# Kernel tuning notes

Measured on AMD Instinct MI355X. Metric: run time of the kernel, lower is better.

Reference implementation:

```python
import jax, jax.numpy as jnp
import numpy as np

NUM_HEADS = 32
ROPE_BASE = 10000.0
MASK_NEG = -66504.0  # from (1 - tril) * -66504.0 in the source


def _rotate_half(x):
    d = x.shape[-1] // 2
    return jnp.concatenate([-x[..., d:], x[..., :d]], axis=-1)


def setup_inputs() -> dict:
    key = jax.random.key(0)
    k1, k2, k3, k4 = jax.random.split(key, 4)
    S, B, E = 2048, 2, 2048
    return {
        "hidden_states": jax.random.normal(k1, (S, B, E), dtype=jnp.float32) * 0.02,
        "qkv_w": jax.random.normal(k2, (E, 3 * E), dtype=jnp.float32) * 0.02,
        "qkv_b": jax.random.normal(k3, (3 * E,), dtype=jnp.float32) * 0.02,
        "out_w": jax.random.normal(k4, (E, E), dtype=jnp.float32) * 0.02,
        "out_b": jnp.zeros((E,), dtype=jnp.float32),
    }


def reference(hidden_states, qkv_w, qkv_b, out_w, out_b):
    # seq-first prompt/prefill path of IPEXTransformerAtten
    S, B, E = hidden_states.shape
    H = NUM_HEADS
    D = E // H

    # fused QKV projection (mm_qkv_out)
    qkv = jnp.einsum('sbe,ef->sbf', hidden_states, qkv_w) + qkv_b  # [S,B,3E]
    q, k, v = jnp.split(qkv, 3, axis=-1)
    q = q.reshape(S, B, H, D)
    k = k.reshape(S, B, H, D)
    v = v.reshape(S, B, H, D)

    # rotary embedding (GPT-NeoX style, full head_dim)
    inv_freq = 1.0 / (ROPE_BASE ** (jnp.arange(0, D, 2, dtype=jnp.float32) / D))
    freqs = jnp.arange(S, dtype=jnp.float32)[:, None] * inv_freq  # [S, D/2]
    emb = jnp.concatenate([freqs, freqs], axis=-1)  # [S, D]
    cos = jnp.cos(emb)[:, None, None, :].astype(hidden_states.dtype)
    sin = jnp.sin(emb)[:, None, None, :].astype(hidden_states.dtype)
    q = q * cos + _rotate_half(q) * sin
    k = k * cos + _rotate_half(k) * sin

    # scaled dot-product attention with causal mask
    scale = 1.0 / jnp.sqrt(jnp.array(D, dtype=hidden_states.dtype))
    scores = jnp.einsum('sbhd,tbhd->bhst', q, k) * scale  # [B,H,S,S]
    causal = jnp.tril(jnp.ones((S, S), dtype=scores.dtype))
    scores = scores + (1.0 - causal) * MASK_NEG
    attn = jax.nn.softmax(scores, axis=-1)
    ctx = jnp.einsum('bhst,tbhd->sbhd', attn, v).reshape(S, B, E)

    # output projection
    return jnp.einsum('sbe,ef->sbf', ctx, out_w) + out_b
```

## Files before the change

### kernel.cpp

```cpp
#include <hip/hip_runtime.h>
#include <hip/hip_bf16.h>

#define S_LEN 2048
#define BATCH 2
#define EMB   2048
#define NH    32
#define HD    64
#define M_ROWS (S_LEN * BATCH)
#define QKV_N  (3 * EMB)

typedef short bf16x8 __attribute__((ext_vector_type(8)));
typedef float f32x4  __attribute__((ext_vector_type(4)));

__device__ __forceinline__ unsigned short f2bf(float f) {
  unsigned int u = __float_as_uint(f);
  u += 0x7fffu + ((u >> 16) & 1u);
  return (unsigned short)(u >> 16);
}
__device__ __forceinline__ float bf2f(unsigned short h) {
  return __uint_as_float(((unsigned int)h) << 16);
}
__device__ __forceinline__ void async_copy16(const void* g, void* lds_d) {
  __builtin_amdgcn_global_load_lds(
      (const __attribute__((address_space(1))) void*)g,
      (__attribute__((address_space(3))) void*)lds_d, 16, 0, 0);
}

#if __has_builtin(__builtin_amdgcn_exp2f)
#define EXP2F(x) __builtin_amdgcn_exp2f(x)
#else
#define EXP2F(x) __expf((x) * 0.6931471805599453f)
#endif


__global__ __launch_bounds__(256) void cast_to_bf16(
    const float* __restrict__ in, unsigned short* __restrict__ out, int n4) {
  int i = blockIdx.x * 256 + threadIdx.x;
  if (i >= n4) return;
  float4 v = reinterpret_cast<const float4*>(in)[i];
  ushort4 o;
  o.x = f2bf(v.x); o.y = f2bf(v.y); o.z = f2bf(v.z); o.w = f2bf(v.w);
  reinterpret_cast<ushort4*>(out)[i] = o;
}

__global__ __launch_bounds__(256) void transpose_cast(
    const float* __restrict__ in, unsigned short* __restrict__ out, int R, int C) {
  __shared__ unsigned short t[64][65];
  const int bc = blockIdx.x * 64, br = blockIdx.y * 64;
  const int tx = threadIdx.x & 63, ty = threadIdx.x >> 6;
  #pragma unroll
  for (int rr = ty; rr < 64; rr += 4)
    t[rr][tx] = f2bf(in[(size_t)(br + rr) * C + bc + tx]);
  __syncthreads();
  #pragma unroll
  for (int rr = ty; rr < 64; rr += 4)
    out[(size_t)(bc + rr) * R + br + tx] = t[tx][rr];
}


constexpr int TILE_SH = 24576;
constexpr int GEMM_LDS_BYTES = 3 * TILE_SH * 2;

__global__ __launch_bounds__(512, 2) void gemm_qkv(
    const unsigned short* __restrict__ A,
    const unsigned short* __restrict__ Wt,
    const float* __restrict__ bias,
    unsigned short* __restrict__ Qo,
    unsigned short* __restrict__ Ko,
    unsigned short* __restrict__ Vo) {
  extern __shared__ unsigned short lds[];
  const int tid = threadIdx.x;
  const int n0 = blockIdx.x * 128;
  const int m0 = blockIdx.y * 256;
  const int wave = tid >> 6, lane = tid & 63;
  const int wm = (wave >> 1) * 64, wn = (wave & 1) * 64;
  const int lm = lane & 15, lq = lane >> 4;
  const int K = 2048;
  const int NT = K / 64;

  const int srow = tid >> 3;
  const int gch  = (tid & 7) ^ (srow & 7);
  const unsigned short* Ab = A  + (size_t)(m0 + srow) * K + gch * 8;
  const unsigned short* Bb = Wt + (size_t)(n0 + srow) * K + gch * 8;

  auto stA = [&](int bufi, int k0, int rep) {
    async_copy16(Ab + (size_t)rep * 64 * K + k0,
                 lds + (size_t)bufi * TILE_SH + ((size_t)rep * 512 + tid) * 8);
  };
  auto stB = [&](int bufi, int k0, int rep) {
    async_copy16(Bb + (size_t)rep * 64 * K + k0,
                 lds + (size_t)bufi * TILE_SH + 16384 + ((size_t)rep * 512 + tid) * 8);
  };

  f32x4 acc[4][4] = {};

  stA(0, 0, 0); stA(0, 0, 1); stA(0, 0, 2); stA(0, 0, 3); stB(0, 0, 0); stB(0, 0, 1);
  stA(1, 64, 0); stA(1, 64, 1); stA(1, 64, 2); stA(1, 64, 3); stB(1, 64, 0); stB(1, 64, 1);
  asm volatile("s_waitcnt vmcnt(6)" ::: "memory");
  __builtin_amdgcn_s_barrier();

  int cur = 0;
  for (int t = 0; t < NT; t++) {
    const unsigned short* Abuf = lds + (size_t)cur * TILE_SH;
    const unsigned short* Bbuf = Abuf + 16384;
    const int pb = (cur >= 1) ? cur - 1 : 2;
    const int pk = (t + 2) * 64;
    const bool pre = (t + 2) < NT;

    bf16x8 b[4][2], a[2][2];
    #pragma unroll
    for (int j = 0; j < 4; j++) {
      const int R = wn + j * 16 + lm;
      #pragma unroll
      for (int ks = 0; ks < 2; ks++)
        b[j][ks] = *reinterpret_cast<const bf16x8*>(
            Bbuf + (size_t)R * 64 + (((ks * 4 + lq) ^ (R & 7)) * 8));
    }
    #pragma unroll
    for (int i = 0; i < 2; i++) {
      const int R = wm + i * 16 + lm;
      #pragma unroll
      for (int ks = 0; ks < 2; ks++)
        a[i][ks] = *reinterpret_cast<const bf16x8*>(
            Abuf + (size_t)R * 64 + (((ks * 4 + lq) ^ (R & 7)) * 8));
    }
    if (pre) { stA(pb, pk, 0); stA(pb, pk, 1); stB(pb, pk, 0); }
    __builtin_amdgcn_s_barrier();
    asm volatile("s_waitcnt lgkmcnt(0)" ::: "memory");
    __builtin_amdgcn_s_setprio(1);
    #pragma unroll
    for (int ks = 0; ks < 2; ks++)
      #pragma unroll
      for (int i = 0; i < 2; i++)
        #pragma unroll
        for (int j = 0; j < 4; j++)
          acc[i][j] = __builtin_amdgcn_mfma_f32_16x16x32_bf16(a[i][ks], b[j][ks], acc[i][j], 0, 0, 0);
    __builtin_amdgcn_s_setprio(0);
    __builtin_amdgcn_s_barrier();

    #pragma unroll
    for (int i = 0; i < 2; i++) {
      const int R = wm + (i + 2) * 16 + lm;
      #pragma unroll
      for (int ks = 0; ks < 2; ks++)
        a[i][ks] = *reinterpret_cast<const bf16x8*>(
            Abuf + (size_t)R * 64 + (((ks * 4 + lq) ^ (R & 7)) * 8));
    }
    if (pre) { stA(pb, pk, 2); stA(pb, pk, 3); stB(pb, pk, 1); }
    __builtin_amdgcn_s_barrier();
    asm volatile("s_waitcnt lgkmcnt(0)" ::: "memory");
    __builtin_amdgcn_s_setprio(1);
    #pragma unroll
    for (int ks = 0; ks < 2; ks++)
      #pragma unroll
      for (int i = 0; i < 2; i++)
        #pragma unroll
        for (int j = 0; j < 4; j++)
          acc[i + 2][j] = __builtin_amdgcn_mfma_f32_16x16x32_bf16(a[i][ks], b[j][ks], acc[i + 2][j], 0, 0, 0);
    __builtin_amdgcn_s_setprio(0);
    if (t + 1 < NT) {
      if (pre) asm volatile("s_waitcnt vmcnt(6)" ::: "memory");
      else     asm volatile("s_waitcnt vmcnt(0)" ::: "memory");
      __builtin_amdgcn_s_barrier();
    }
    cur = (cur == 2) ? 0 : cur + 1;
  }

  const int which = n0 >> 11;
  unsigned short* dst = (which == 0) ? Qo : (which == 1) ? Ko : Vo;
  float bv[4];
  #pragma unroll
  for (int j = 0; j < 4; j++) bv[j] = bias[n0 + wn + j * 16 + lm];

  if (which < 2) {
    #pragma unroll
    for (int j = 0; j < 2; j++) {
      const int n = n0 + wn + j * 16 + lm;
      const int e = n & (EMB - 1), h = e >> 6, d = e & 63;
      const float invf = EXP2F((float)d * -0.4152410118609203f);
      #pragma unroll
      for (int i = 0; i < 4; i++) {
        #pragma unroll
        for (int r = 0; r < 4; r++) {
          const int m = m0 + wm + i * 16 + lq * 4 + r;
          const int s = m >> 1, b = m & 1;
          const float v1 = acc[i][j][r]     + bv[j];
          const float v2 = acc[i][j + 2][r] + bv[j + 2];
          float sn, cs;
          __sincosf((float)s * invf, &sn, &cs);
          const size_t base = (((size_t)b * NH + h) * S_LEN + s) * HD + d;
          dst[base]      = f2bf(v1 * cs - v2 * sn);
          dst[base + 32] = f2bf(v2 * cs + v1 * sn);
        }
      }
    }
  } else {
    #pragma unroll
    for (int j = 0; j < 4; j++) {
      const int n = n0 + wn + j * 16 + lm;
      const int e = n & (EMB - 1), h = e >> 6, d = e & 63;
      #pragma unroll
      for (int i = 0; i < 4; i++) {
        #pragma unroll
        for (int r = 0; r < 4; r++) {
          const int m = m0 + wm + i * 16 + lq * 4 + r;
          const int s = m >> 1, b = m & 1;
          dst[(((size_t)b * NH + h) * S_LEN + s) * HD + d] = f2bf(acc[i][j][r] + bv[j]);
        }
      }
    }
  }
}


__global__ __launch_bounds__(256) void transpose_v(
    const unsigned short* __restrict__ V, unsigned short* __restrict__ VT) {
  __shared__ unsigned short t[64][65];
  const int bh = blockIdx.y;
  const int s0 = blockIdx.x * 64;
  const int tx = threadIdx.x & 63, ty = threadIdx.x >> 6;
  const unsigned short* src = V + ((size_t)bh * S_LEN + s0) * HD;
  #pragma unroll
  for (int r = ty; r < 64; r += 4)
    t[r][tx] = src[(size_t)r * HD + tx];
  __syncthreads();
  unsigned short* dst = VT + (size_t)bh * HD * S_LEN + s0;
  #pragma unroll
  for (int r = ty; r < 64; r += 4)
    dst[(size_t)r * S_LEN + tx] = t[tx][r];
}


__global__ __launch_bounds__(256) void attn_kernel(
    const unsigned short* __restrict__ Q,
    const unsigned short* __restrict__ K,
    const unsigned short* __restrict__ VT,
    unsigned short* __restrict__ ctx) {
  const int bh = blockIdx.x;
  const int p  = blockIdx.y;
  const int tid = threadIdx.x;
  const int wave = tid >> 6, lane = tid & 63;
  const int lm = lane & 15, lq = lane >> 4;
  const int b = bh >> 5, h = bh & 31;
  const char* Qb8 = (const char*)(Q  + (size_t)bh * S_LEN * HD);
  const char* Kb8 = (const char*)(K  + (size_t)bh * S_LEN * HD);
  const char* Vb8 = (const char*)(VT + (size_t)bh * HD * S_LEN);

  __shared__ __align__(16) unsigned short Ks[2][2][64][32];
  __shared__ __align__(16) unsigned short Pbuf[4][32][72];
  unsigned short* Pw = &Pbuf[wave][0][0];

  const float C = 0.18033688011112042f;
  const int q0A = p * 128, q0B = (15 - p) * 128;
  const int r0A = q0A + wave * 32, r0B = q0B + wave * 32;
  const int nt = (q0B >> 6) + 2;

  const int srw = tid >> 2, sc16 = (tid & 3) * 16;

  bf16x8 qf[2][2][2];
  #pragma unroll
  for (int s = 0; s < 2; s++) {
    const int rr = (s == 0) ? r0A : r0B;
    #pragma unroll
    for (int i = 0; i < 2; i++)
      #pragma unroll
      for (int ks = 0; ks < 2; ks++)
        qf[s][i][ks] = *reinterpret_cast<const bf16x8*>(
            Qb8 + (size_t)(rr + i*16 + lm) * 128 + ks*64 + lq*16);
  }

  f32x4 O[2][2][4] = {};
  float l[2][2][4] = {};

  {
    char* kd = (char*)&Ks[0][0][0][0];
    async_copy16(Kb8 + (size_t)srw * 128      + sc16, kd        + tid*16);
    async_copy16(Kb8 + (size_t)srw * 128 + 64 + sc16, kd + 4096 + tid*16);
  }
  __syncthreads();

  for (int t = 0; t < nt; t++) {
    const int t0 = t * 64;
    const int buf = t & 1;

    if (t + 1 < nt) {
      const int t1 = t0 + 64;
      char* kd = (char*)&Ks[buf ^ 1][0][0][0];
      async_copy16(Kb8 + (size_t)(t1 + srw) * 128      + sc16, kd        + tid*16);
      async_copy16(Kb8 + (size_t)(t1 + srw) * 128 + 64 + sc16, kd + 4096 + tid*16);
    }

    const char* KsB = (const char*)&Ks[buf][0][0][0];

    #pragma unroll
    for (int s = 0; s < 2; s++) {
      const int rr = (s == 0) ? r0A : r0B;
      if (t0 <= rr + 31) {
        const bool clean = (t0 + 63 <= rr);
        const int jmax  = clean ? 4 : ((rr == t0) ? 2 : 4);
        const int kslim = clean ? 2 : ((rr == t0) ? 1 : 2);
        const int srow_c = rr + lq * 4;

        f32x4 sc[2][4] = {};
        #pragma unroll
        for (int ks = 0; ks < 2; ks++) {
          bf16x8 kf[4];
          #pragma unroll
          for (int j = 0; j < 4; j++)
            if (j < jmax)
              kf[j] = *reinterpret_cast<const bf16x8*>(
                  KsB + ks*4096 + (j*16 + lm)*64 + lq*16);
          #pragma unroll
          for (int i = 0; i < 2; i++)
            #pragma unroll
            for (int j = 0; j < 4; j++)
              if (j < jmax)
                sc[i][j] = __builtin_amdgcn_mfma_f32_16x16x32_bf16(
                    qf[s][i][ks], kf[j], sc[i][j], 0, 0, 0);
        }

        if (clean) {
          #pragma unroll
          for (int i = 0; i < 2; i++)
            #pragma unroll
            for (int j = 0; j < 4; j++)
              #pragma unroll
              for (int r = 0; r < 4; r++) {
                const float pe = EXP2F(sc[i][j][r] * C);
                l[s][i][r] += pe;
                Pw[(i*16 + lq*4 + r) * 72 + j*16 + lm] = f2bf(pe);
              }
        } else {
          #pragma unroll
          for (int i = 0; i < 2; i++)
            #pragma unroll
            for (int j = 0; j < 4; j++)
              if (j < jmax)
                #pragma unroll
                for (int r = 0; r < 4; r++) {
                  const int srow = srow_c + i*16 + r;
                  const int tcol = t0 + j*16 + lm;
                  const float pe = (tcol <= srow) ? EXP2F(sc[i][j][r] * C) : 0.0f;
                  l[s][i][r] += pe;
                  Pw[(i*16 + lq*4 + r) * 72 + j*16 + lm] = f2bf(pe);
                }
        }

        #pragma unroll
        for (int ks = 0; ks < 2; ks++) {
          if (ks < kslim) {
            bf16x8 pf[2], vf[4];
            #pragma unroll
            for (int i = 0; i < 2; i++)
              pf[i] = *reinterpret_cast<const bf16x8*>(Pw + (i*16 + lm)*72 + ks*32 + lq*8);
            #pragma unroll
            for (int j = 0; j < 4; j++)
              vf[j] = *reinterpret_cast<const bf16x8*>(
                  Vb8 + (size_t)(j*16 + lm) * 4096 + t0*2 + ks*64 + lq*16);
            #pragma unroll
            for (int i = 0; i < 2; i++)
              #pragma unroll
              for (int j = 0; j < 4; j++)
                O[s][i][j] = __builtin_amdgcn_mfma_f32_16x16x32_bf16(
                    pf[i], vf[j], O[s][i][j], 0, 0, 0);
          }
        }
      }
    }
    __syncthreads();
  }

  #pragma unroll
  for (int s = 0; s < 2; s++) {
    const int rr = (s == 0) ? r0A : r0B;
    #pragma unroll
    for (int i = 0; i < 2; i++) {
      #pragma unroll
      for (int r = 0; r < 4; r++) {
        float sum = l[s][i][r];
        sum += __shfl_xor(sum, 1, 64);
        sum += __shfl_xor(sum, 2, 64);
        sum += __shfl_xor(sum, 4, 64);
        sum += __shfl_xor(sum, 8, 64);
        const float inv = 1.0f / sum;
        const int srow = rr + lq*4 + i*16 + r;
        #pragma unroll
        for (int j = 0; j < 4; j++) {
          const int d = j*16 + lm;
          ctx[((size_t)srow * BATCH + b) * EMB + h*HD + d] = f2bf(O[s][i][j][r] * inv);
        }
      }
    }
  }
}


__global__ __launch_bounds__(512, 2) void gemm_out(
    const unsigned short* __restrict__ A,
    const unsigned short* __restrict__ Wt,
    const float* __restrict__ bias,
    float* __restrict__ out) {
  extern __shared__ unsigned short lds[];
  const int tid = threadIdx.x;
  const int n0 = blockIdx.x * 128;
  const int m0 = blockIdx.y * 256;
  const int wave = tid >> 6, lane = tid & 63;
  const int wm = (wave >> 1) * 64, wn = (wave & 1) * 64;
  const int lm = lane & 15, lq = lane >> 4;
  const int K = 2048;
  const int NT = K / 64;

  const int srow = tid >> 3;
  const int gch  = (tid & 7) ^ (srow & 7);
  const unsigned short* Ab = A  + (size_t)(m0 + srow) * K + gch * 8;
  const unsigned short* Bb = Wt + (size_t)(n0 + srow) * K + gch * 8;

  auto stA = [&](int bufi, int k0, int rep) {
    async_copy16(Ab + (size_t)rep * 64 * K + k0,
                 lds + (size_t)bufi * TILE_SH + ((size_t)rep * 512 + tid) * 8);
  };
  auto stB = [&](int bufi, int k0, int rep) {
    async_copy16(Bb + (size_t)rep * 64 * K + k0,
                 lds + (size_t)bufi * TILE_SH + 16384 + ((size_t)rep * 512 + tid) * 8);
  };

  f32x4 acc[4][4] = {};

  stA(0, 0, 0); stA(0, 0, 1); stA(0, 0, 2); stA(0, 0, 3); stB(0, 0, 0); stB(0, 0, 1);
  stA(1, 64, 0); stA(1, 64, 1); stA(1, 64, 2); stA(1, 64, 3); stB(1, 64, 0); stB(1, 64, 1);
  asm volatile("s_waitcnt vmcnt(6)" ::: "memory");
  __builtin_amdgcn_s_barrier();

  int cur = 0;
  for (int t = 0; t < NT; t++) {
    const unsigned short* Abuf = lds + (size_t)cur * TILE_SH;
    const unsigned short* Bbuf = Abuf + 16384;
    const int pb = (cur >= 1) ? cur - 1 : 2;
    const int pk = (t + 2) * 64;
    const bool pre = (t + 2) < NT;

    bf16x8 b[4][2], a[2][2];
    #pragma unroll
    for (int j = 0; j < 4; j++) {
      const int R = wn + j * 16 + lm;
      #pragma unroll
      for (int ks = 0; ks < 2; ks++)
        b[j][ks] = *reinterpret_cast<const bf16x8*>(
            Bbuf + (size_t)R * 64 + (((ks * 4 + lq) ^ (R & 7)) * 8));
    }
    #pragma unroll
    for (int i = 0; i < 2; i++) {
      const int R = wm + i * 16 + lm;
      #pragma unroll
      for (int ks = 0; ks < 2; ks++)
        a[i][ks] = *reinterpret_cast<const bf16x8*>(
            Abuf + (size_t)R * 64 + (((ks * 4 + lq) ^ (R & 7)) * 8));
    }
    if (pre) { stA(pb, pk, 0); stA(pb, pk, 1); stB(pb, pk, 0); }
    __builtin_amdgcn_s_barrier();
    asm volatile("s_waitcnt lgkmcnt(0)" ::: "memory");
    __builtin_amdgcn_s_setprio(1);
    #pragma unroll
    for (int ks = 0; ks < 2; ks++)
      #pragma unroll
      for (int i = 0; i < 2; i++)
        #pragma unroll
        for (int j = 0; j < 4; j++)
          acc[i][j] = __builtin_amdgcn_mfma_f32_16x16x32_bf16(a[i][ks], b[j][ks], acc[i][j], 0, 0, 0);
    __builtin_amdgcn_s_setprio(0);
    __builtin_amdgcn_s_barrier();

    #pragma unroll
    for (int i = 0; i < 2; i++) {
      const int R = wm + (i + 2) * 16 + lm;
      #pragma unroll
      for (int ks = 0; ks < 2; ks++)
        a[i][ks] = *reinterpret_cast<const bf16x8*>(
            Abuf + (size_t)R * 64 + (((ks * 4 + lq) ^ (R & 7)) * 8));
    }
    if (pre) { stA(pb, pk, 2); stA(pb, pk, 3); stB(pb, pk, 1); }
    __builtin_amdgcn_s_barrier();
    asm volatile("s_waitcnt lgkmcnt(0)" ::: "memory");
    __builtin_amdgcn_s_setprio(1);
    #pragma unroll
    for (int ks = 0; ks < 2; ks++)
      #pragma unroll
      for (int i = 0; i < 2; i++)
        #pragma unroll
        for (int j = 0; j < 4; j++)
          acc[i + 2][j] = __builtin_amdgcn_mfma_f32_16x16x32_bf16(a[i][ks], b[j][ks], acc[i + 2][j], 0, 0, 0);
    __builtin_amdgcn_s_setprio(0);
    if (t + 1 < NT) {
      if (pre) asm volatile("s_waitcnt vmcnt(6)" ::: "memory");
      else     asm volatile("s_waitcnt vmcnt(0)" ::: "memory");
      __builtin_amdgcn_s_barrier();
    }
    cur = (cur == 2) ? 0 : cur + 1;
  }

  #pragma unroll
  for (int j = 0; j < 4; j++) {
    const int n = n0 + wn + j * 16 + lm;
    const float bv = bias[n];
    #pragma unroll
    for (int i = 0; i < 4; i++) {
      #pragma unroll
      for (int r = 0; r < 4; r++) {
        const int m = m0 + wm + i * 16 + lq * 4 + r;
        out[(size_t)m * EMB + n] = acc[i][j][r] + bv;
      }
    }
  }
}


extern "C" void kernel_launch(void* const* d_in, const int* in_sizes, int n_in,
                              void* d_out, int out_size, void* d_ws, size_t ws_size,
                              hipStream_t stream) {
  const float* hidden = (const float*)d_in[0];
  const float* qkv_w  = (const float*)d_in[1];
  const float* qkv_b  = (const float*)d_in[2];
  const float* out_w  = (const float*)d_in[3];
  const float* out_b  = (const float*)d_in[4];
  float* out = (float*)d_out;

  static bool attr_set = false;
  if (!attr_set) {
    hipFuncSetAttribute(reinterpret_cast<const void*>(gemm_qkv),
                        hipFuncAttributeMaxDynamicSharedMemorySize, GEMM_LDS_BYTES);
    hipFuncSetAttribute(reinterpret_cast<const void*>(gemm_out),
                        hipFuncAttributeMaxDynamicSharedMemorySize, GEMM_LDS_BYTES);
    attr_set = true;
  }

  unsigned short* ws = (unsigned short*)d_ws;
  unsigned short* hbf   = ws;
  unsigned short* qkvwT = hbf   + (size_t)M_ROWS * EMB;
  unsigned short* outwT = qkvwT + (size_t)QKV_N * EMB;
  unsigned short* Qb    = outwT + (size_t)EMB * EMB;
  unsigned short* Kb    = Qb    + (size_t)64 * S_LEN * HD;
  unsigned short* Vb    = Kb    + (size_t)64 * S_LEN * HD;
  unsigned short* VTb   = Vb    + (size_t)64 * S_LEN * HD;
  unsigned short* ctx   = VTb   + (size_t)64 * S_LEN * HD;

  cast_to_bf16<<<(M_ROWS * EMB / 4) / 256, 256, 0, stream>>>(hidden, hbf, M_ROWS * EMB / 4);
  transpose_cast<<<dim3(QKV_N / 64, EMB / 64), 256, 0, stream>>>(qkv_w, qkvwT, EMB, QKV_N);
  transpose_cast<<<dim3(EMB / 64, EMB / 64), 256, 0, stream>>>(out_w, outwT, EMB, EMB);

  gemm_qkv<<<dim3(QKV_N / 128, M_ROWS / 256), 512, GEMM_LDS_BYTES, stream>>>(
      hbf, qkvwT, qkv_b, Qb, Kb, Vb);

  transpose_v<<<dim3(S_LEN / 64, 64), 256, 0, stream>>>(Vb, VTb);

  attn_kernel<<<dim3(64, 8), 256, 0, stream>>>(Qb, Kb, VTb, ctx);

  gemm_out<<<dim3(EMB / 128, M_ROWS / 256), 512, GEMM_LDS_BYTES, stream>>>(
      ctx, outwT, out_b, out);
}
```

Measured before the change: 399.9 us.

## Merge prep kernels, write V transposed from QKV GEMM, stage V in LDS

The three preprocessing launches (hidden cast and two weight transpose-casts) become one kernel that dispatches on block index. The QKV GEMM epilogue now transposes its V tile through LDS and writes V^T directly, which removes the separate transpose_v kernel and its intermediate V buffer round trip. The attention kernel double-buffers V^T tiles into LDS with async copies alongside K, instead of reading V fragments straight from global memory. This cuts launch overhead and global traffic at the cost of more LDS per attention block and an extra barrier in the GEMM epilogue.

Result: faster. 361.1 us, median of 3 (-9.7%).

```diff
diff --git a/kernel.cpp b/kernel.cpp
--- a/kernel.cpp
+++ b/kernel.cpp
@@ -33,21 +33,19 @@
 #endif
 
 
-__global__ __launch_bounds__(256) void cast_to_bf16(
-    const float* __restrict__ in, unsigned short* __restrict__ out, int n4) {
-  int i = blockIdx.x * 256 + threadIdx.x;
-  if (i >= n4) return;
-  float4 v = reinterpret_cast<const float4*>(in)[i];
-  ushort4 o;
-  o.x = f2bf(v.x); o.y = f2bf(v.y); o.z = f2bf(v.z); o.w = f2bf(v.w);
-  reinterpret_cast<ushort4*>(out)[i] = o;
-}
-
-__global__ __launch_bounds__(256) void transpose_cast(
-    const float* __restrict__ in, unsigned short* __restrict__ out, int R, int C) {
+#define CAST_BLKS  (M_ROWS * EMB / 4 / 256)
+#define TCQ_BX     (QKV_N / 64)
+#define TCQ_BLKS   (TCQ_BX * (EMB / 64))
+#define TCO_BX     (EMB / 64)
+#define TCO_BLKS   (TCO_BX * (EMB / 64))
+#define PREP_BLKS  (CAST_BLKS + TCQ_BLKS + TCO_BLKS)
+
+__device__ __forceinline__ void transpose_body(
+    const float* __restrict__ in, unsigned short* __restrict__ out,
+    int R, int C, int bx, int by, int tid) {
   __shared__ unsigned short t[64][65];
-  const int bc = blockIdx.x * 64, br = blockIdx.y * 64;
-  const int tx = threadIdx.x & 63, ty = threadIdx.x >> 6;
+  const int bc = bx * 64, br = by * 64;
+  const int tx = tid & 63, ty = tid >> 6;
   #pragma unroll
   for (int rr = ty; rr < 64; rr += 4)
     t[rr][tx] = f2bf(in[(size_t)(br + rr) * C + bc + tx]);
@@ -57,6 +55,26 @@
     out[(size_t)(bc + rr) * R + br + tx] = t[tx][rr];
 }
 
+__global__ __launch_bounds__(256) void prep_all(
+    const float* __restrict__ hidden, unsigned short* __restrict__ hbf,
+    const float* __restrict__ qkv_w, unsigned short* __restrict__ qkvwT,
+    const float* __restrict__ out_w, unsigned short* __restrict__ outwT) {
+  const int bid = blockIdx.x, tid = threadIdx.x;
+  if (bid < CAST_BLKS) {
+    const int i = bid * 256 + tid;
+    float4 v = reinterpret_cast<const float4*>(hidden)[i];
+    ushort4 o;
+    o.x = f2bf(v.x); o.y = f2bf(v.y); o.z = f2bf(v.z); o.w = f2bf(v.w);
+    reinterpret_cast<ushort4*>(hbf)[i] = o;
+  } else if (bid < CAST_BLKS + TCQ_BLKS) {
+    const int b = bid - CAST_BLKS;
+    transpose_body(qkv_w, qkvwT, EMB, QKV_N, b % TCQ_BX, b / TCQ_BX, tid);
+  } else {
+    const int b = bid - CAST_BLKS - TCQ_BLKS;
+    transpose_body(out_w, outwT, EMB, EMB, b % TCO_BX, b / TCO_BX, tid);
+  }
+}
+
 
 constexpr int TILE_SH = 24576;
 constexpr int GEMM_LDS_BYTES = 3 * TILE_SH * 2;
@@ -67,7 +85,7 @@
     const float* __restrict__ bias,
     unsigned short* __restrict__ Qo,
     unsigned short* __restrict__ Ko,
-    unsigned short* __restrict__ Vo) {
+    unsigned short* __restrict__ VTo) {
   extern __shared__ unsigned short lds[];
   const int tid = threadIdx.x;
   const int n0 = blockIdx.x * 128;
@@ -167,12 +185,12 @@
   }
 
   const int which = n0 >> 11;
-  unsigned short* dst = (which == 0) ? Qo : (which == 1) ? Ko : Vo;
   float bv[4];
   #pragma unroll
   for (int j = 0; j < 4; j++) bv[j] = bias[n0 + wn + j * 16 + lm];
 
   if (which < 2) {
+    unsigned short* dst = (which == 0) ? Qo : Ko;
     #pragma unroll
     for (int j = 0; j < 2; j++) {
       const int n = n0 + wn + j * 16 + lm;
@@ -195,39 +213,33 @@
       }
     }
   } else {
+    __syncthreads();
+    unsigned short* T = lds;
     #pragma unroll
     for (int j = 0; j < 4; j++) {
-      const int n = n0 + wn + j * 16 + lm;
-      const int e = n & (EMB - 1), h = e >> 6, d = e & 63;
+      const int nl = wn + j * 16 + lm;
       #pragma unroll
       for (int i = 0; i < 4; i++) {
-        #pragma unroll
-        for (int r = 0; r < 4; r++) {
-          const int m = m0 + wm + i * 16 + lq * 4 + r;
-          const int s = m >> 1, b = m & 1;
-          dst[(((size_t)b * NH + h) * S_LEN + s) * HD + d] = f2bf(acc[i][j][r] + bv[j]);
-        }
+        const int sbase = (wm >> 1) + i * 8 + lq * 2;
+        #pragma unroll
+        for (int r = 0; r < 4; r++)
+          T[nl * 264 + (r & 1) * 128 + sbase + (r >> 1)] = f2bf(acc[i][j][r] + bv[j]);
       }
     }
-  }
-}
-
-
-__global__ __launch_bounds__(256) void transpose_v(
-    const unsigned short* __restrict__ V, unsigned short* __restrict__ VT) {
-  __shared__ unsigned short t[64][65];
-  const int bh = blockIdx.y;
-  const int s0 = blockIdx.x * 64;
-  const int tx = threadIdx.x & 63, ty = threadIdx.x >> 6;
-  const unsigned short* src = V + ((size_t)bh * S_LEN + s0) * HD;
-  #pragma unroll
-  for (int r = ty; r < 64; r += 4)
-    t[r][tx] = src[(size_t)r * HD + tx];
-  __syncthreads();
-  unsigned short* dst = VT + (size_t)bh * HD * S_LEN + s0;
-  #pragma unroll
-  for (int r = ty; r < 64; r += 4)
-    dst[(size_t)r * S_LEN + tx] = t[tx][r];
+    __syncthreads();
+    const int h0 = (n0 & (EMB - 1)) >> 6;
+    const int s0 = m0 >> 1;
+    #pragma unroll
+    for (int k = 0; k < 8; k++) {
+      const int c = k * 512 + tid;
+      const int row = c >> 4, ch = c & 15;
+      const int nl = row >> 1, bb = row & 1;
+      const bf16x8 v = *reinterpret_cast<const bf16x8*>(T + nl * 264 + bb * 128 + ch * 8);
+      const int hh = h0 + (nl >> 6), d = nl & 63;
+      *reinterpret_cast<bf16x8*>(
+          VTo + (((size_t)bb * NH + hh) * HD + d) * S_LEN + s0 + ch * 8) = v;
+    }
+  }
 }
 
 
@@ -247,6 +259,7 @@
   const char* Vb8 = (const char*)(VT + (size_t)bh * HD * S_LEN);
 
   __shared__ __align__(16) unsigned short Ks[2][2][64][32];
+  __shared__ __align__(16) unsigned short Vs[2][2][64][32];
   __shared__ __align__(16) unsigned short Pbuf[4][32][72];
   unsigned short* Pw = &Pbuf[wave][0][0];
 
@@ -274,8 +287,11 @@
 
   {
     char* kd = (char*)&Ks[0][0][0][0];
+    char* vd = (char*)&Vs[0][0][0][0];
     async_copy16(Kb8 + (size_t)srw * 128      + sc16, kd        + tid*16);
     async_copy16(Kb8 + (size_t)srw * 128 + 64 + sc16, kd + 4096 + tid*16);
+    async_copy16(Vb8 + (size_t)srw * 4096      + sc16, vd        + tid*16);
+    async_copy16(Vb8 + (size_t)srw * 4096 + 64 + sc16, vd + 4096 + tid*16);
   }
   __syncthreads();
 
@@ -286,11 +302,15 @@
     if (t + 1 < nt) {
       const int t1 = t0 + 64;
       char* kd = (char*)&Ks[buf ^ 1][0][0][0];
+      char* vd = (char*)&Vs[buf ^ 1][0][0][0];
       async_copy16(Kb8 + (size_t)(t1 + srw) * 128      + sc16, kd        + tid*16);
       async_copy16(Kb8 + (size_t)(t1 + srw) * 128 + 64 + sc16, kd + 4096 + tid*16);
+      async_copy16(Vb8 + (size_t)srw * 4096 + t1*2      + sc16, vd        + tid*16);
+      async_copy16(Vb8 + (size_t)srw * 4096 + t1*2 + 64 + sc16, vd + 4096 + tid*16);
     }
 
     const char* KsB = (const char*)&Ks[buf][0][0][0];
+    const char* VsB = (const char*)&Vs[buf][0][0][0];
 
     #pragma unroll
     for (int s = 0; s < 2; s++) {
@@ -356,7 +376,7 @@
             #pragma unroll
             for (int j = 0; j < 4; j++)
               vf[j] = *reinterpret_cast<const bf16x8*>(
-                  Vb8 + (size_t)(j*16 + lm) * 4096 + t0*2 + ks*64 + lq*16);
+                  VsB + ks*4096 + (j*16 + lm)*64 + lq*16);
             #pragma unroll
             for (int i = 0; i < 2; i++)
               #pragma unroll
@@ -539,18 +559,13 @@
   unsigned short* outwT = qkvwT + (size_t)QKV_N * EMB;
   unsigned short* Qb    = outwT + (size_t)EMB * EMB;
   unsigned short* Kb    = Qb    + (size_t)64 * S_LEN * HD;
-  unsigned short* Vb    = Kb    + (size_t)64 * S_LEN * HD;
-  unsigned short* VTb   = Vb    + (size_t)64 * S_LEN * HD;
+  unsigned short* VTb   = Kb    + (size_t)64 * S_LEN * HD;
   unsigned short* ctx   = VTb   + (size_t)64 * S_LEN * HD;
 
-  cast_to_bf16<<<(M_ROWS * EMB / 4) / 256, 256, 0, stream>>>(hidden, hbf, M_ROWS * EMB / 4);
-  transpose_cast<<<dim3(QKV_N / 64, EMB / 64), 256, 0, stream>>>(qkv_w, qkvwT, EMB, QKV_N);
-  transpose_cast<<<dim3(EMB / 64, EMB / 64), 256, 0, stream>>>(out_w, outwT, EMB, EMB);
+  prep_all<<<PREP_BLKS, 256, 0, stream>>>(hidden, hbf, qkv_w, qkvwT, out_w, outwT);
 
   gemm_qkv<<<dim3(QKV_N / 128, M_ROWS / 256), 512, GEMM_LDS_BYTES, stream>>>(
-      hbf, qkvwT, qkv_b, Qb, Kb, Vb);
-
-  transpose_v<<<dim3(S_LEN / 64, 64), 256, 0, stream>>>(Vb, VTb);
+      hbf, qkvwT, qkv_b, Qb, Kb, VTb);
 
   attn_kernel<<<dim3(64, 8), 256, 0, stream>>>(Qb, Kb, VTb, ctx);
 
```
